# Kernel optimization log

Hardware: AMD Instinct MI355X
Metric: run time of the kernel (lower is better)

The kernel has to match this reference:

```python
import jax, jax.numpy as jnp
import numpy as np

D_EMBED = 1024


def setup_inputs() -> dict:
    key = jax.random.key(0)
    ks = jax.random.split(key, 8)
    B, S, D = 8, 2048, D_EMBED
    scale = 1.0 / np.sqrt(D)
    return {
        "embeddings": jax.random.normal(ks[0], (B, S, D), dtype=jnp.float32),
        "mask": jnp.zeros((B, S, S), dtype=jnp.float32),
        "Wq": jax.random.normal(ks[1], (D, D), dtype=jnp.float32) * scale,
        "bq": jax.random.normal(ks[2], (D,), dtype=jnp.float32) * 0.02,
        "Wk": jax.random.normal(ks[3], (D, D), dtype=jnp.float32) * scale,
        "bk": jax.random.normal(ks[4], (D,), dtype=jnp.float32) * 0.02,
        "Wv": jax.random.normal(ks[5], (D, D), dtype=jnp.float32) * scale,
        "bv": jax.random.normal(ks[6], (D,), dtype=jnp.float32) * 0.02,
    }


def reference(embeddings, mask, Wq, bq, Wk, bk, Wv, bv):
    # torch Linear: y = x @ W.T + b
    q = jnp.einsum('bsd,ed->bse', embeddings, Wq) + bq
    k = jnp.einsum('bsd,ed->bse', embeddings, Wk) + bk
    v = jnp.einsum('bsd,ed->bse', embeddings, Wv) + bv
    scores = jnp.einsum('bqd,bkd->bqk', q, k)
    # NOTE: faithful to source — mask added BEFORE scaling by 1/sqrt(d)
    scores = (scores + mask) * (1.0 / jnp.sqrt(jnp.float32(q.shape[-1])))
    attn = jax.nn.softmax(scores, axis=-1)
    return jnp.einsum('bqk,bkd->bqd', attn, v)
```

## Files before the change

### kernel.cpp

```cpp
#include <hip/hip_runtime.h>


#define B_SZ 8
#define SEQ  2048
#define DIM  1024
#define MROWS (B_SZ * SEQ)

typedef unsigned short u16;
typedef short short8 __attribute__((ext_vector_type(8)));
typedef unsigned short u16x4 __attribute__((ext_vector_type(4)));
typedef float f32x4 __attribute__((ext_vector_type(4)));

__device__ __forceinline__ u16 f2h(float x) {
  _Float16 h = (_Float16)x;
  union { _Float16 f; u16 u; } c; c.f = h; return c.u;
}
__device__ __forceinline__ float h2f(u16 u) {
  union { _Float16 f; u16 u; } c; c.u = u; return (float)c.f;
}

__device__ __forceinline__ int xcd_swz(int x, int nwg) {
  return (x & 7) * (nwg >> 3) + (x >> 3);
}

__device__ __forceinline__ void gload_lds16(const u16* g, u16* l) {
  __builtin_amdgcn_global_load_lds(
      (__attribute__((address_space(1))) void*)(g),
      (__attribute__((address_space(3))) void*)(l), 16, 0, 0);
}

__device__ __forceinline__ f32x4 mfma_f16(short8 a, short8 b, f32x4 c) {
  asm("v_mfma_f32_16x16x32_f16 %0, %1, %2, %0" : "+v"(c) : "v"(a), "v"(b));
  return c;
}

__device__ __forceinline__ void gemm256_core(const u16* __restrict__ Ag,
                                             const u16* __restrict__ Bg,
                                             int NT, size_t lda, size_t ldb,
                                             u16* sm, f32x4 (&acc)[8][4]) {
  const int tid = threadIdx.x;
  const int lane = tid & 63;
  const int wid = tid >> 6;
  const int wm = wid >> 2;
  const int wn = wid & 3;
  const int wm8 = wm << 3;
  const int wn4 = wn << 2;

  u16* sA = sm;
  u16* sB = sm + 32768;

  const int bb = (lane << 4) ^ (((lane >> 5) & 1) << 5);
  const int rins = bb >> 6;
  const int cins = (bb & 63) >> 1;
  const int s0 = wid, s1 = 8 + wid, s2 = 16 + wid, s3 = 24 + wid;
  const size_t aoff0 = (size_t)((s0 >> 1) * 16 + rins) * lda + ((s0 & 1) * 32 + cins);
  const size_t aoff1 = (size_t)((s1 >> 1) * 16 + rins) * lda + ((s1 & 1) * 32 + cins);
  const size_t aoff2 = (size_t)((s2 >> 1) * 16 + rins) * lda + ((s2 & 1) * 32 + cins);
  const size_t aoff3 = (size_t)((s3 >> 1) * 16 + rins) * lda + ((s3 & 1) * 32 + cins);
  const size_t boff0 = (size_t)((s0 >> 1) * 16 + rins) * ldb + ((s0 & 1) * 32 + cins);
  const size_t boff1 = (size_t)((s1 >> 1) * 16 + rins) * ldb + ((s1 & 1) * 32 + cins);
  const size_t boff2 = (size_t)((s2 >> 1) * 16 + rins) * ldb + ((s2 & 1) * 32 + cins);
  const size_t boff3 = (size_t)((s3 >> 1) * 16 + rins) * ldb + ((s3 & 1) * 32 + cins);
  const int wid512 = wid << 9;

  const int lof = ((lane & 15) << 6) + ((lane >> 4) << 4);
  const int loe = (lof ^ (((lane >> 3) & 1) << 5)) >> 1;

#define ISSUE_A(j, nb, kt) \
  gload_lds16(Ag + aoff##j + (size_t)(kt) * 64, sA + (nb) * 16384 + (j) * 4096 + wid512)
#define ISSUE_B(j, nb, kt) \
  gload_lds16(Bg + boff##j + (size_t)(kt) * 64, sB + (nb) * 16384 + (j) * 4096 + wid512)

  ISSUE_B(0, 0, 0); ISSUE_B(1, 0, 0); ISSUE_B(2, 0, 0); ISSUE_B(3, 0, 0);
  ISSUE_A(0, 0, 0); ISSUE_A(2, 0, 0); ISSUE_A(1, 0, 0); ISSUE_A(3, 0, 0);

  int buf = 0;
  for (int kt = 0; kt < NT; ++kt) {
    const int nk = kt + 1;
    const bool pre = nk < NT;
    const int nb = buf ^ 1;
    asm volatile("s_waitcnt vmcnt(2)" ::: "memory");
    __builtin_amdgcn_s_barrier();
    asm volatile("" ::: "memory");
    const u16* bufA = sA + buf * 16384;
    const u16* bufB = sB + buf * 16384;
    short8 bf[4][2];
#pragma unroll
    for (int n = 0; n < 4; ++n) {
      bf[n][0] = *(const short8*)(bufB + (wn4 + n) * 1024 + loe);
      bf[n][1] = *(const short8*)(bufB + (wn4 + n) * 1024 + 512 + loe);
    }
    {
      short8 af[2][2];
#pragma unroll
      for (int m = 0; m < 2; ++m) {
        af[m][0] = *(const short8*)(bufA + (wm8 + m) * 1024 + loe);
        af[m][1] = *(const short8*)(bufA + (wm8 + m) * 1024 + 512 + loe);
      }
      if (pre) {
        ISSUE_B(0, nb, nk); ISSUE_B(1, nb, nk); ISSUE_B(2, nb, nk); ISSUE_B(3, nb, nk);
        ISSUE_A(0, nb, nk); ISSUE_A(2, nb, nk); ISSUE_A(1, nb, nk); ISSUE_A(3, nb, nk);
      }
      __builtin_amdgcn_s_setprio(1);
#pragma unroll
      for (int m = 0; m < 2; ++m)
#pragma unroll
        for (int n = 0; n < 4; ++n) {
          acc[m][n] = mfma_f16(af[m][0], bf[n][0], acc[m][n]);
          acc[m][n] = mfma_f16(af[m][1], bf[n][1], acc[m][n]);
        }
      __builtin_amdgcn_s_setprio(0);
    }
    {
      short8 af[2][2];
#pragma unroll
      for (int m = 0; m < 2; ++m) {
        af[m][0] = *(const short8*)(bufA + (wm8 + 2 + m) * 1024 + loe);
        af[m][1] = *(const short8*)(bufA + (wm8 + 2 + m) * 1024 + 512 + loe);
      }
      __builtin_amdgcn_s_setprio(1);
#pragma unroll
      for (int m = 0; m < 2; ++m)
#pragma unroll
        for (int n = 0; n < 4; ++n) {
          acc[2 + m][n] = mfma_f16(af[m][0], bf[n][0], acc[2 + m][n]);
          acc[2 + m][n] = mfma_f16(af[m][1], bf[n][1], acc[2 + m][n]);
        }
      __builtin_amdgcn_s_setprio(0);
    }
    if (pre) {
      asm volatile("s_waitcnt vmcnt(8)" ::: "memory");
    } else {
      asm volatile("s_waitcnt vmcnt(0)" ::: "memory");
    }
    __builtin_amdgcn_s_barrier();
    asm volatile("" ::: "memory");
    {
      short8 af[2][2];
#pragma unroll
      for (int m = 0; m < 2; ++m) {
        af[m][0] = *(const short8*)(bufA + (wm8 + 4 + m) * 1024 + loe);
        af[m][1] = *(const short8*)(bufA + (wm8 + 4 + m) * 1024 + 512 + loe);
      }
      __builtin_amdgcn_s_setprio(1);
#pragma unroll
      for (int m = 0; m < 2; ++m)
#pragma unroll
        for (int n = 0; n < 4; ++n) {
          acc[4 + m][n] = mfma_f16(af[m][0], bf[n][0], acc[4 + m][n]);
          acc[4 + m][n] = mfma_f16(af[m][1], bf[n][1], acc[4 + m][n]);
        }
      __builtin_amdgcn_s_setprio(0);
    }
    {
      short8 af[2][2];
#pragma unroll
      for (int m = 0; m < 2; ++m) {
        af[m][0] = *(const short8*)(bufA + (wm8 + 6 + m) * 1024 + loe);
        af[m][1] = *(const short8*)(bufA + (wm8 + 6 + m) * 1024 + 512 + loe);
      }
      __builtin_amdgcn_s_setprio(1);
#pragma unroll
      for (int m = 0; m < 2; ++m)
#pragma unroll
        for (int n = 0; n < 4; ++n) {
          acc[6 + m][n] = mfma_f16(af[m][0], bf[n][0], acc[6 + m][n]);
          acc[6 + m][n] = mfma_f16(af[m][1], bf[n][1], acc[6 + m][n]);
        }
      __builtin_amdgcn_s_setprio(0);
    }
    buf ^= 1;
  }
  asm volatile("s_nop 7\n\ts_nop 7\n\ts_nop 7" ::);
#undef ISSUE_A
#undef ISSUE_B
}

__global__ __launch_bounds__(256) void cvt_kernel(const float* __restrict__ in,
                                                  u16* __restrict__ out, int n4) {
  int i = blockIdx.x * 256 + threadIdx.x;
  if (i >= n4) return;
  float4 v = ((const float4*)in)[i];
  u16x4 o;
  o[0] = f2h(v.x); o[1] = f2h(v.y); o[2] = f2h(v.z); o[3] = f2h(v.w);
  ((u16x4*)out)[i] = o;
}

__global__ __launch_bounds__(256) void cvt_w3_kernel(const float* __restrict__ Wq,
                                                     const float* __restrict__ Wk,
                                                     const float* __restrict__ Wv,
                                                     u16* __restrict__ B3) {
  int b = blockIdx.x;
  int w = b >> 10;
  int i = (b & 1023) * 256 + threadIdx.x;
  const float* src = (w == 0) ? Wq : (w == 1) ? Wk : Wv;
  float4 v = ((const float4*)src)[i];
  u16x4 o;
  o[0] = f2h(v.x); o[1] = f2h(v.y); o[2] = f2h(v.z); o[3] = f2h(v.w);
  ((u16x4*)(B3 + (size_t)w * DIM * DIM))[i] = o;
}

__global__ __launch_bounds__(512) void proj256_kernel(const u16* __restrict__ emb16,
                                                      const u16* __restrict__ B3,
                                                      const float* __restrict__ bq,
                                                      const float* __restrict__ bk,
                                                      const float* __restrict__ bv,
                                                      u16* __restrict__ q16,
                                                      u16* __restrict__ k16,
                                                      u16* __restrict__ vT) {
  __shared__ __align__(16) u16 sm[65536];
  const int wg = xcd_swz(blockIdx.x, 768);
  const int lane = threadIdx.x & 63, wid = threadIdx.x >> 6;
  f32x4 acc[8][4] = {};
  if (wg < 512) {
    const int m0 = (wg >> 3) * 256;
    const int z = (wg >> 2) & 1;
    const int n0 = (wg & 3) * 256;
    gemm256_core(emb16 + (size_t)m0 * 1024, B3 + (size_t)z * DIM * DIM + (size_t)n0 * 1024,
                 16, 1024, 1024, sm, acc);
    const int rb = m0 + ((wid >> 2) << 7) + ((lane >> 4) << 2);
    const int cb = n0 + ((wid & 3) << 6) + (lane & 15);
    const float* bias = z ? bk : bq;
    u16* dst = z ? k16 : q16;
#pragma unroll
    for (int m = 0; m < 8; ++m)
#pragma unroll
      for (int n = 0; n < 4; ++n)
#pragma unroll
        for (int j = 0; j < 4; ++j) {
          int row = rb + m * 16 + j;
          int col = cb + n * 16;
          dst[(size_t)row * DIM + col] = f2h(acc[m][n][j] + bias[col]);
        }
  } else {
    const int r = wg - 512;
    const int m0 = (r & 3) * 256;
    const int n0 = (r >> 2) * 256;
    gemm256_core(B3 + (size_t)2 * DIM * DIM + (size_t)m0 * 1024, emb16 + (size_t)n0 * 1024,
                 16, 1024, 1024, sm, acc);
    const int rb = m0 + ((wid >> 2) << 7) + ((lane >> 4) << 2);
    const int cb = n0 + ((wid & 3) << 6) + (lane & 15);
#pragma unroll
    for (int m = 0; m < 8; ++m)
#pragma unroll
      for (int n = 0; n < 4; ++n)
#pragma unroll
        for (int j = 0; j < 4; ++j) {
          int d = rb + m * 16 + j;
          int kg = cb + n * 16;
          int bi = kg >> 11, s = kg & 2047;
          vT[((size_t)bi << 21) + ((size_t)d << 11) + s] = f2h(acc[m][n][j] + bv[d]);
        }
  }
}

__global__ __launch_bounds__(512) void scores256_kernel(const u16* __restrict__ q16,
                                                        const u16* __restrict__ k16,
                                                        u16* __restrict__ scH) {
  __shared__ __align__(16) u16 sm[65536];
  const int wg = xcd_swz(blockIdx.x, 512);
  const int b = wg >> 6;
  const int m0 = ((wg >> 3) & 7) * 256;
  const int n0 = (wg & 7) * 256;
  f32x4 acc[8][4] = {};
  gemm256_core(q16 + ((size_t)b * SEQ + m0) * DIM, k16 + ((size_t)b * SEQ + n0) * DIM,
               16, DIM, DIM, sm, acc);
  const int lane = threadIdx.x & 63, wid = threadIdx.x >> 6;
  const int rb = m0 + ((wid >> 2) << 7) + ((lane >> 4) << 2);
  const int cb = n0 + ((wid & 3) << 6) + (lane & 15);
#pragma unroll
  for (int m = 0; m < 8; ++m)
#pragma unroll
    for (int n = 0; n < 4; ++n)
#pragma unroll
      for (int j = 0; j < 4; ++j) {
        size_t idx = ((size_t)b * SEQ + rb + m * 16 + j) * SEQ + (cb + n * 16);
        scH[idx] = f2h(acc[m][n][j] * 0.03125f);
      }
}

__global__ __launch_bounds__(256) void softmax_kernel(u16* __restrict__ scH,
                                                      const float* __restrict__ mask) {
  __shared__ float red[8];
  const size_t row = blockIdx.x;
  u16* rowp = scH + row * SEQ;
  const float* mrow = mask + row * SEQ;
  const int tid = threadIdx.x;
  short8 raw = *(const short8*)(rowp + tid * 8);
  float4 m0 = ((const float4*)mrow)[2 * tid];
  float4 m1 = ((const float4*)mrow)[2 * tid + 1];
  float mk[8] = {m0.x, m0.y, m0.z, m0.w, m1.x, m1.y, m1.z, m1.w};
  float f[8];
#pragma unroll
  for (int j = 0; j < 8; ++j) f[j] = h2f((u16)raw[j]) + mk[j] * 0.03125f;
  float mx = f[0];
#pragma unroll
  for (int j = 1; j < 8; ++j) mx = fmaxf(mx, f[j]);
#pragma unroll
  for (int off = 1; off < 64; off <<= 1) mx = fmaxf(mx, __shfl_xor(mx, off));
  const int wid = tid >> 6, lane = tid & 63;
  if (lane == 0) red[wid] = mx;
  __syncthreads();
  mx = fmaxf(fmaxf(red[0], red[1]), fmaxf(red[2], red[3]));
  float e[8];
  float s = 0.f;
#pragma unroll
  for (int j = 0; j < 8; ++j) {
    e[j] = __expf(f[j] - mx);
    s += e[j];
  }
#pragma unroll
  for (int off = 1; off < 64; off <<= 1) s += __shfl_xor(s, off);
  if (lane == 0) red[4 + wid] = s;
  __syncthreads();
  s = (red[4] + red[5]) + (red[6] + red[7]);
  const float inv = 1.f / s;
  short8 o;
#pragma unroll
  for (int j = 0; j < 8; ++j) o[j] = (short)f2h(e[j] * inv);
  *(short8*)(rowp + tid * 8) = o;
}

__global__ __launch_bounds__(512) void pv256_kernel(const u16* __restrict__ pr,
                                                    const u16* __restrict__ vt,
                                                    float* __restrict__ out) {
  __shared__ __align__(16) u16 sm[65536];
  const int wg = xcd_swz(blockIdx.x, 256);
  const int b = wg >> 5;
  const int m0 = ((wg >> 2) & 7) * 256;
  const int n0 = (wg & 3) * 256;
  f32x4 acc[8][4] = {};
  gemm256_core(pr + ((size_t)b * SEQ + m0) * SEQ, vt + ((size_t)b * DIM + n0) * SEQ,
               32, SEQ, SEQ, sm, acc);
  const int lane = threadIdx.x & 63, wid = threadIdx.x >> 6;
  const int rb = m0 + ((wid >> 2) << 7) + ((lane >> 4) << 2);
  const int cb = n0 + ((wid & 3) << 6) + (lane & 15);
#pragma unroll
  for (int m = 0; m < 8; ++m)
#pragma unroll
    for (int n = 0; n < 4; ++n)
#pragma unroll
      for (int j = 0; j < 4; ++j)
        out[((size_t)b * SEQ + rb + m * 16 + j) * DIM + (cb + n * 16)] = acc[m][n][j];
}

extern "C" void kernel_launch(void* const* d_in, const int* in_sizes, int n_in,
                              void* d_out, int out_size, void* d_ws, size_t ws_size,
                              hipStream_t stream) {
  const float* emb  = (const float*)d_in[0];
  const float* mask = (const float*)d_in[1];
  const float* Wq   = (const float*)d_in[2];
  const float* bq   = (const float*)d_in[3];
  const float* Wk   = (const float*)d_in[4];
  const float* bk   = (const float*)d_in[5];
  const float* Wv   = (const float*)d_in[6];
  const float* bv   = (const float*)d_in[7];
  float* out = (float*)d_out;

  const size_t M1 = 1024 * 1024;
  u16* scH   = (u16*)d_ws;
  u16* emb16 = scH + 32 * M1;
  u16* B3  = emb16 + 16 * M1;
  u16* q16 = B3 + 3 * M1;
  u16* k16 = q16 + 16 * M1;
  u16* vT  = k16 + 16 * M1;

  cvt_kernel<<<16384, 256, 0, stream>>>(emb, emb16, (int)(4 * M1));
  cvt_w3_kernel<<<3072, 256, 0, stream>>>(Wq, Wk, Wv, B3);

  proj256_kernel<<<768, 512, 0, stream>>>(emb16, B3, bq, bk, bv, q16, k16, vT);

  scores256_kernel<<<512, 512, 0, stream>>>(q16, k16, scH);
  softmax_kernel<<<MROWS, 256, 0, stream>>>(scH, mask);
  pv256_kernel<<<256, 512, 0, stream>>>((const u16*)scH, vT, out);
}
```

Baseline: 312.0 us.

## Fold Wq and Wk into one matrix to drop the Q/K projections

Rewrites scores as X·(Wq^T Wk)·X^T plus per-key bias terms. Query-only terms cancel in the softmax, and the key-side bias term is precomputed through small GEMM and dot-product kernels. This removes one of the two 16384x1024x1024 projection GEMMs, replacing Q and K with a single G = X·M projection, at the cost of several tiny extra launches. It also rounds the fused matrix to fp16, which can change numerical accuracy.

```diff
diff --git a/kernel.cpp b/kernel.cpp
--- a/kernel.cpp
+++ b/kernel.cpp
@@ -41,10 +41,8 @@
   const int tid = threadIdx.x;
   const int lane = tid & 63;
   const int wid = tid >> 6;
-  const int wm = wid >> 2;
-  const int wn = wid & 3;
-  const int wm8 = wm << 3;
-  const int wn4 = wn << 2;
+  const int wm8 = (wid >> 2) << 3;
+  const int wn4 = (wid & 3) << 2;
 
   u16* sA = sm;
   u16* sB = sm + 32768;
@@ -176,6 +174,49 @@
 #undef ISSUE_B
 }
 
+__device__ __forceinline__ void gemm128_core(const u16* A, const u16* Bt, int K,
+                                             int lda, int ldb, f32x4 (&acc)[4][4],
+                                             u16* sA, u16* sB) {
+  const int tid = threadIdx.x;
+  const int lane = tid & 63;
+  const int wid = tid >> 6;
+  const int wr = wid >> 1;
+  const int wc = wid & 1;
+  const int srow = tid >> 2;
+  const int scol = (tid & 3) << 3;
+  const u16* ga0 = A + (size_t)srow * lda + scol;
+  const u16* ga1 = A + (size_t)(srow + 64) * lda + scol;
+  const u16* gb0 = Bt + (size_t)srow * ldb + scol;
+  const u16* gb1 = Bt + (size_t)(srow + 64) * ldb + scol;
+  u16* la0 = sA + (wid << 9);
+  u16* la1 = sA + 2048 + (wid << 9);
+  u16* lb0 = sB + (wid << 9);
+  u16* lb1 = sB + 2048 + (wid << 9);
+  const u16* pa = sA + (size_t)((wr << 6) + (lane & 15)) * 32 + ((lane >> 4) << 3);
+  const u16* pb = sB + (size_t)((wc << 6) + (lane & 15)) * 32 + ((lane >> 4) << 3);
+  const int ksteps = K >> 5;
+  for (int kt = 0; kt < ksteps; ++kt) {
+    gload_lds16(ga0, la0);
+    gload_lds16(ga1, la1);
+    gload_lds16(gb0, lb0);
+    gload_lds16(gb1, lb1);
+    ga0 += 32; ga1 += 32; gb0 += 32; gb1 += 32;
+    __syncthreads();
+    short8 a[4], b[4];
+#pragma unroll
+    for (int i = 0; i < 4; ++i) a[i] = *(const short8*)(pa + (i << 9));
+#pragma unroll
+    for (int i = 0; i < 4; ++i) b[i] = *(const short8*)(pb + (i << 9));
+#pragma unroll
+    for (int mi = 0; mi < 4; ++mi)
+#pragma unroll
+      for (int ni = 0; ni < 4; ++ni)
+        acc[mi][ni] = mfma_f16(a[mi], b[ni], acc[mi][ni]);
+    __syncthreads();
+  }
+  asm volatile("s_nop 7\n\ts_nop 7\n\ts_nop 7" ::);
+}
+
 __global__ __launch_bounds__(256) void cvt_kernel(const float* __restrict__ in,
                                                   u16* __restrict__ out, int n4) {
   int i = blockIdx.x * 256 + threadIdx.x;
@@ -186,58 +227,125 @@
   ((u16x4*)out)[i] = o;
 }
 
-__global__ __launch_bounds__(256) void cvt_w3_kernel(const float* __restrict__ Wq,
+__global__ __launch_bounds__(256) void cvt_wT_kernel(const float* __restrict__ Wq,
                                                      const float* __restrict__ Wk,
-                                                     const float* __restrict__ Wv,
-                                                     u16* __restrict__ B3) {
-  int b = blockIdx.x;
-  int w = b >> 10;
-  int i = (b & 1023) * 256 + threadIdx.x;
-  const float* src = (w == 0) ? Wq : (w == 1) ? Wk : Wv;
-  float4 v = ((const float4*)src)[i];
-  u16x4 o;
-  o[0] = f2h(v.x); o[1] = f2h(v.y); o[2] = f2h(v.z); o[3] = f2h(v.w);
-  ((u16x4*)(B3 + (size_t)w * DIM * DIM))[i] = o;
+                                                     u16* __restrict__ WqT,
+                                                     u16* __restrict__ WkT) {
+  __shared__ float t[64][65];
+  const float* src = blockIdx.z ? Wk : Wq;
+  u16* dst = blockIdx.z ? WkT : WqT;
+  const int r0 = blockIdx.x * 64;
+  const int c0 = blockIdx.y * 64;
+  const int tid = threadIdx.x;
+  const int tr = tid >> 4;
+  const int c4 = (tid & 15) << 2;
+#pragma unroll
+  for (int i = 0; i < 4; ++i) {
+    float4 x = *(const float4*)(src + (size_t)(r0 + tr + 16 * i) * 1024 + c0 + c4);
+    t[tr + 16 * i][c4 + 0] = x.x;
+    t[tr + 16 * i][c4 + 1] = x.y;
+    t[tr + 16 * i][c4 + 2] = x.z;
+    t[tr + 16 * i][c4 + 3] = x.w;
+  }
+  __syncthreads();
+#pragma unroll
+  for (int i = 0; i < 4; ++i) {
+    int dr = tr + 16 * i;
+    u16x4 y;
+    y[0] = f2h(t[c4 + 0][dr]);
+    y[1] = f2h(t[c4 + 1][dr]);
+    y[2] = f2h(t[c4 + 2][dr]);
+    y[3] = f2h(t[c4 + 3][dr]);
+    *(u16x4*)(dst + (size_t)(c0 + dr) * 1024 + r0 + c4) = y;
+  }
+}
+
+__global__ __launch_bounds__(256) void mtw_kernel(const u16* __restrict__ WqT,
+                                                  const u16* __restrict__ WkT,
+                                                  const float* __restrict__ bq,
+                                                  u16* __restrict__ Mt,
+                                                  float* __restrict__ w) {
+  __shared__ __align__(16) u16 sA[128 * 32];
+  __shared__ __align__(16) u16 sB[128 * 32];
+  const int b = blockIdx.x;
+  if (b < 64) {
+    const int m0 = (b >> 3) * 128;
+    const int n0 = (b & 7) * 128;
+    f32x4 acc[4][4] = {};
+    gemm128_core(WkT + (size_t)m0 * 1024, WqT + (size_t)n0 * 1024, 1024, 1024, 1024,
+                 acc, sA, sB);
+    const int lane = threadIdx.x & 63, wid = threadIdx.x >> 6;
+    const int wr = wid >> 1, wc = wid & 1;
+#pragma unroll
+    for (int mi = 0; mi < 4; ++mi)
+#pragma unroll
+      for (int ni = 0; ni < 4; ++ni)
+#pragma unroll
+        for (int j = 0; j < 4; ++j) {
+          int row = m0 + (wr << 6) + mi * 16 + ((lane >> 4) << 2) + j;
+          int col = n0 + (wc << 6) + ni * 16 + (lane & 15);
+          Mt[(size_t)row * 1024 + col] = f2h(acc[mi][ni][j] * 0.03125f);
+        }
+  } else {
+    const int e = (b - 64) * 256 + threadIdx.x;
+    const u16* row = WkT + (size_t)e * 1024;
+    float s = 0.f;
+    for (int d = 0; d < 1024; d += 8) {
+      short8 v = *(const short8*)(row + d);
+#pragma unroll
+      for (int j = 0; j < 8; ++j) s += h2f((u16)v[j]) * bq[d + j];
+    }
+    w[e] = s * 0.03125f;
+  }
+}
+
+__global__ __launch_bounds__(256) void c_kernel(const u16* __restrict__ emb16,
+                                                const float* __restrict__ w,
+                                                float* __restrict__ c) {
+  __shared__ float sw[1024];
+  for (int i = threadIdx.x; i < 1024; i += 256) sw[i] = w[i];
+  __syncthreads();
+  const int r = blockIdx.x * 256 + threadIdx.x;
+  const u16* row = emb16 + (size_t)r * 1024;
+  float s = 0.f;
+  for (int d = 0; d < 1024; d += 8) {
+    short8 v = *(const short8*)(row + d);
+#pragma unroll
+    for (int j = 0; j < 8; ++j) s += h2f((u16)v[j]) * sw[d + j];
+  }
+  c[r] = s;
 }
 
 __global__ __launch_bounds__(512) void proj256_kernel(const u16* __restrict__ emb16,
-                                                      const u16* __restrict__ B3,
-                                                      const float* __restrict__ bq,
-                                                      const float* __restrict__ bk,
+                                                      const u16* __restrict__ Mt,
+                                                      const u16* __restrict__ Wv16,
                                                       const float* __restrict__ bv,
-                                                      u16* __restrict__ q16,
-                                                      u16* __restrict__ k16,
+                                                      u16* __restrict__ G,
                                                       u16* __restrict__ vT) {
   __shared__ __align__(16) u16 sm[65536];
-  const int wg = xcd_swz(blockIdx.x, 768);
+  const int wg = xcd_swz(blockIdx.x, 512);
   const int lane = threadIdx.x & 63, wid = threadIdx.x >> 6;
   f32x4 acc[8][4] = {};
-  if (wg < 512) {
-    const int m0 = (wg >> 3) * 256;
-    const int z = (wg >> 2) & 1;
+  if (wg < 256) {
+    const int m0 = (wg >> 2) * 256;
     const int n0 = (wg & 3) * 256;
-    gemm256_core(emb16 + (size_t)m0 * 1024, B3 + (size_t)z * DIM * DIM + (size_t)n0 * 1024,
-                 16, 1024, 1024, sm, acc);
+    gemm256_core(emb16 + (size_t)m0 * 1024, Mt + (size_t)n0 * 1024, 16, 1024, 1024,
+                 sm, acc);
     const int rb = m0 + ((wid >> 2) << 7) + ((lane >> 4) << 2);
     const int cb = n0 + ((wid & 3) << 6) + (lane & 15);
-    const float* bias = z ? bk : bq;
-    u16* dst = z ? k16 : q16;
 #pragma unroll
     for (int m = 0; m < 8; ++m)
 #pragma unroll
       for (int n = 0; n < 4; ++n)
 #pragma unroll
-        for (int j = 0; j < 4; ++j) {
-          int row = rb + m * 16 + j;
-          int col = cb + n * 16;
-          dst[(size_t)row * DIM + col] = f2h(acc[m][n][j] + bias[col]);
-        }
+        for (int j = 0; j < 4; ++j)
+          G[(size_t)(rb + m * 16 + j) * 1024 + (cb + n * 16)] = f2h(acc[m][n][j]);
   } else {
-    const int r = wg - 512;
+    const int r = wg - 256;
     const int m0 = (r & 3) * 256;
     const int n0 = (r >> 2) * 256;
-    gemm256_core(B3 + (size_t)2 * DIM * DIM + (size_t)m0 * 1024, emb16 + (size_t)n0 * 1024,
-                 16, 1024, 1024, sm, acc);
+    gemm256_core(Wv16 + (size_t)m0 * 1024, emb16 + (size_t)n0 * 1024, 16, 1024, 1024,
+                 sm, acc);
     const int rb = m0 + ((wid >> 2) << 7) + ((lane >> 4) << 2);
     const int cb = n0 + ((wid & 3) << 6) + (lane & 15);
 #pragma unroll
@@ -254,8 +362,9 @@
   }
 }
 
-__global__ __launch_bounds__(512) void scores256_kernel(const u16* __restrict__ q16,
-                                                        const u16* __restrict__ k16,
+__global__ __launch_bounds__(512) void scores256_kernel(const u16* __restrict__ G,
+                                                        const u16* __restrict__ emb16,
+                                                        const float* __restrict__ c,
                                                         u16* __restrict__ scH) {
   __shared__ __align__(16) u16 sm[65536];
   const int wg = xcd_swz(blockIdx.x, 512);
@@ -263,11 +372,14 @@
   const int m0 = ((wg >> 3) & 7) * 256;
   const int n0 = (wg & 7) * 256;
   f32x4 acc[8][4] = {};
-  gemm256_core(q16 + ((size_t)b * SEQ + m0) * DIM, k16 + ((size_t)b * SEQ + n0) * DIM,
+  gemm256_core(G + ((size_t)b * SEQ + m0) * DIM, emb16 + ((size_t)b * SEQ + n0) * DIM,
                16, DIM, DIM, sm, acc);
   const int lane = threadIdx.x & 63, wid = threadIdx.x >> 6;
   const int rb = m0 + ((wid >> 2) << 7) + ((lane >> 4) << 2);
   const int cb = n0 + ((wid & 3) << 6) + (lane & 15);
+  float cn[4];
+#pragma unroll
+  for (int n = 0; n < 4; ++n) cn[n] = c[(size_t)b * SEQ + cb + n * 16];
 #pragma unroll
   for (int m = 0; m < 8; ++m)
 #pragma unroll
@@ -275,7 +387,7 @@
 #pragma unroll
       for (int j = 0; j < 4; ++j) {
         size_t idx = ((size_t)b * SEQ + rb + m * 16 + j) * SEQ + (cb + n * 16);
-        scH[idx] = f2h(acc[m][n][j] * 0.03125f);
+        scH[idx] = f2h(acc[m][n][j] + cn[n]);
       }
 }
 
@@ -356,21 +468,30 @@
   const float* Wv   = (const float*)d_in[6];
   const float* bv   = (const float*)d_in[7];
   float* out = (float*)d_out;
+  (void)bk;
 
   const size_t M1 = 1024 * 1024;
   u16* scH   = (u16*)d_ws;
   u16* emb16 = scH + 32 * M1;
-  u16* B3  = emb16 + 16 * M1;
-  u16* q16 = B3 + 3 * M1;
-  u16* k16 = q16 + 16 * M1;
-  u16* vT  = k16 + 16 * M1;
+  u16* WqT   = emb16 + 16 * M1;
+  u16* WkT   = WqT + M1;
+  u16* Wv16  = WkT + M1;
+  u16* Mt    = Wv16 + M1;
+  u16* G     = Mt + M1;
+  u16* vT    = G + 16 * M1;
+  float* w   = (float*)(vT + 16 * M1);
+  float* c   = w + 1024;
 
   cvt_kernel<<<16384, 256, 0, stream>>>(emb, emb16, (int)(4 * M1));
-  cvt_w3_kernel<<<3072, 256, 0, stream>>>(Wq, Wk, Wv, B3);
-
-  proj256_kernel<<<768, 512, 0, stream>>>(emb16, B3, bq, bk, bv, q16, k16, vT);
-
-  scores256_kernel<<<512, 512, 0, stream>>>(q16, k16, scH);
+  cvt_wT_kernel<<<dim3(16, 16, 2), 256, 0, stream>>>(Wq, Wk, WqT, WkT);
+  cvt_kernel<<<1024, 256, 0, stream>>>(Wv, Wv16, (int)(M1 / 4));
+
+  mtw_kernel<<<68, 256, 0, stream>>>(WqT, WkT, bq, Mt, w);
+  c_kernel<<<64, 256, 0, stream>>>(emb16, w, c);
+
+  proj256_kernel<<<512, 512, 0, stream>>>(emb16, Mt, Wv16, bv, G, vT);
+
+  scores256_kernel<<<512, 512, 0, stream>>>(G, emb16, c, scH);
   softmax_kernel<<<MROWS, 256, 0, stream>>>(scH, mask);
   pv256_kernel<<<256, 512, 0, stream>>>((const u16*)scH, vT, out);
 }
```

After: 335.0 us. 7.4% more time.
